# Optimization experiments

Hardware: AMD Instinct MI355X
Metric: run time of the kernel (lower is better)

## Reference

```python
import jax, jax.numpy as jnp
import numpy as np

EPS = 1e-05
NEG = -1e9

def rotate_half(x):
    x1, x2 = jnp.split(x, 2, axis=-1)
    return jnp.concatenate([-x2, x1], axis=-1)

def rmsnorm(x, w):
    xf = x.astype(jnp.float32)
    n = xf * jax.lax.rsqrt(jnp.mean(xf * xf, axis=-1, keepdims=True) + EPS)
    return w * n.astype(x.dtype)

def setup_inputs() -> dict:
    key = jax.random.key(0)
    ks = jax.random.split(key, 12)
    B, S, H, NH, DH, FF = 1, 2048, 2048, 16, 128, 8192
    x = jax.random.normal(ks[0], (B, S, H), jnp.float32)
    # additive causal mask [1,1,S,S]
    causal = jnp.where(jnp.tril(jnp.ones((S, S), bool)), 0.0, NEG).astype(jnp.float32)
    attention_mask = causal[None, None]
    alibi = 0.1 * jax.random.normal(ks[1], (1, NH, S, S), jnp.float32)
    # rotary angles [S, DH]
    inv = 1.0 / (10000.0 ** (jnp.arange(0, DH, 2, dtype=jnp.float32) / DH))
    ang = jnp.arange(S, dtype=jnp.float32)[:, None] * inv[None, :]
    freqs = jnp.concatenate([ang, ang], axis=-1)  # [S, DH]
    sc = 1.0 / np.sqrt(H)
    wq = sc * jax.random.normal(ks[2], (H, H), jnp.float32)
    wk = sc * jax.random.normal(ks[3], (H, H), jnp.float32)
    wv = sc * jax.random.normal(ks[4], (H, H), jnp.float32)
    wo = sc * jax.random.normal(ks[5], (H, H), jnp.float32)
    w1 = sc * jax.random.normal(ks[6], (H, FF), jnp.float32)
    w3 = sc * jax.random.normal(ks[7], (H, FF), jnp.float32)
    w2 = (1.0 / np.sqrt(FF)) * jax.random.normal(ks[8], (FF, H), jnp.float32)
    attn_norm_w = jnp.ones((H,), jnp.float32)
    ffn_norm_w = jnp.ones((H,), jnp.float32)
    return dict(x=x, attention_mask=attention_mask, alibi=alibi, freqs=freqs,
                wq=wq, wk=wk, wv=wv, wo=wo, w1=w1, w2=w2, w3=w3,
                attn_norm_w=attn_norm_w, ffn_norm_w=ffn_norm_w)

def reference(x, attention_mask, alibi, freqs, wq, wk, wv, wo, w1, w2, w3,
              attn_norm_w, ffn_norm_w):
    B, S, H = x.shape
    NH = 16
    DH = H // NH
    nx = rmsnorm(x, attn_norm_w)
    # projections -> [B, NH, S, DH]
    def heads(y):
        return y.reshape(B, S, NH, DH).transpose(0, 2, 1, 3)
    q = heads(nx @ wq)
    k = heads(nx @ wk)
    v = heads(nx @ wv)
    cos, sin = jnp.cos(freqs), jnp.sin(freqs)  # [S, DH] broadcasts over B,NH
    q = q * cos + rotate_half(q) * sin
    k = k * cos + rotate_half(k) * sin
    scores = jnp.einsum('bhqd,bhkd->bhqk', q, k) / np.sqrt(DH)
    scores = scores + attention_mask + alibi
    attn = jax.nn.softmax(scores, axis=-1)
    out = jnp.einsum('bhqk,bhkd->bhqd', attn, v)
    out = out.transpose(0, 2, 1, 3).reshape(B, S, H)
    x = x + out @ wo
    nx = rmsnorm(x, ffn_norm_w)
    ff = (jax.nn.silu(nx @ w1) * (nx @ w3)) @ w2
    return x + ff
```

## Files before the change

### kernel.cpp

```cpp
#include <hip/hip_runtime.h>
#include <hip/hip_bf16.h>
#include <math.h>

typedef __bf16 bf16x8 __attribute__((ext_vector_type(8)));
typedef float  f32x4  __attribute__((ext_vector_type(4)));
typedef unsigned short u16x8 __attribute__((ext_vector_type(8)));
typedef unsigned short u16x4 __attribute__((ext_vector_type(4)));

#define DEV static __device__ __forceinline__

DEV void gload16(const void* g, void* l) {
  __builtin_amdgcn_global_load_lds((__attribute__((address_space(1))) void*)g,
                                   (__attribute__((address_space(3))) void*)l,
                                   16, 0, 0);
}

DEV float bf2f(unsigned short u) {
  unsigned v = ((unsigned)u) << 16;
  return __builtin_bit_cast(float, v);
}
DEV unsigned short f2bf(float f) {
  unsigned u = __builtin_bit_cast(unsigned, f);
  u = u + 0x7fffu + ((u >> 16) & 1u);
  return (unsigned short)(u >> 16);
}

__global__ __launch_bounds__(256) void rmsnorm_k(const float* __restrict__ x,
    const float* __restrict__ w, unsigned short* __restrict__ out, int H) {
  int row = blockIdx.x;
  const float4* xr = (const float4*)(x + (size_t)row * H);
  float4 a = xr[threadIdx.x * 2], b = xr[threadIdx.x * 2 + 1];
  float ss = a.x*a.x + a.y*a.y + a.z*a.z + a.w*a.w
           + b.x*b.x + b.y*b.y + b.z*b.z + b.w*b.w;
#pragma unroll
  for (int o = 32; o; o >>= 1) ss += __shfl_down(ss, o, 64);
  __shared__ float red[4];
  if ((threadIdx.x & 63) == 0) red[threadIdx.x >> 6] = ss;
  __syncthreads();
  float rs = rsqrtf((red[0] + red[1] + red[2] + red[3]) * (1.0f / 2048.0f) + 1e-5f);
  size_t base = (size_t)row * H + threadIdx.x * 8;
  const float* wv = w + threadIdx.x * 8;
  float vals[8] = {a.x, a.y, a.z, a.w, b.x, b.y, b.z, b.w};
  u16x8 o8;
#pragma unroll
  for (int i = 0; i < 8; ++i) o8[i] = f2bf(vals[i] * rs * wv[i]);
  *(u16x8*)(out + base) = o8;
}

__global__ __launch_bounds__(256) void wtrans64_k(const float* __restrict__ W,
    unsigned short* __restrict__ Wt, int R, int C, int ilv) {
  __shared__ unsigned short tile[64][68];
  const int c0 = blockIdx.x * 64, r0 = blockIdx.y * 64;
  const int t = threadIdx.x;
  const int lr = t >> 4, lc4 = (t & 15) * 4;
#pragma unroll
  for (int i = 0; i < 4; ++i) {
    float4 v = *(const float4*)&W[(size_t)(r0 + lr + i * 16) * C + c0 + lc4];
    u16x4 s4;
    s4[0] = f2bf(v.x); s4[1] = f2bf(v.y); s4[2] = f2bf(v.z); s4[3] = f2bf(v.w);
    *(u16x4*)&tile[lr + i * 16][lc4] = s4;
  }
  __syncthreads();
  const int oc = t >> 3, seg = (t & 7) * 8;
#pragma unroll
  for (int i = 0; i < 2; ++i) {
    int c = c0 + oc + i * 32;
    u16x8 o8;
#pragma unroll
    for (int j = 0; j < 8; ++j) o8[j] = tile[seg + j][oc + i * 32];
    size_t dstrow = (ilv < 0) ? (size_t)c
                              : (size_t)(c >> 4) * 32 + (c & 15) + ilv * 16;
    *(u16x8*)&Wt[dstrow * R + r0 + seg] = o8;
  }
}


#define STG_A(H, BUF, KC) do {                                                 \
    gload16(Asrc0 + (size_t)(H) * 128 * lda + (KC),                            \
            &lds[(BUF) * 16384 + (H) * 8192 + w * 1024]);                      \
    gload16(Asrc1 + (size_t)(H) * 128 * lda + (KC),                            \
            &lds[(BUF) * 16384 + (H) * 8192 + w * 1024 + 512]);                \
  } while (0)

#define STG_B(H, BUF, KC) do {                                                 \
    gload16(Bsrc0 + (size_t)(H) * 128 * ldb + (KC),                            \
            &lds[32768 + (BUF) * 16384 + (H) * 8192 + w * 1024]);              \
    gload16(Bsrc1 + (size_t)(H) * 128 * ldb + (KC),                            \
            &lds[32768 + (BUF) * 16384 + (H) * 8192 + w * 1024 + 512]);        \
  } while (0)

#define DS_A(DST, MH) do {                                                     \
    const int abase = buf * 16384 + (MH) * 8192 + arow * 64;                   \
    _Pragma("unroll") for (int m = 0; m < 4; ++m) {                            \
      DST[m][0] = *(const bf16x8*)&lds[abase + m * 1024 + acol0];              \
      DST[m][1] = *(const bf16x8*)&lds[abase + m * 1024 + acol1];              \
    } } while (0)

#define DS_B(DST, NH) do {                                                     \
    const int bbase = 32768 + buf * 16384 + (NH) * 8192 + brow * 64;           \
    _Pragma("unroll") for (int n = 0; n < 2; ++n) {                            \
      DST[n][0] = *(const bf16x8*)&lds[bbase + n * 1024 + acol0];              \
      DST[n][1] = *(const bf16x8*)&lds[bbase + n * 1024 + acol1];              \
    } } while (0)

#define MFMA16(AI, AR, BR) do {                                                \
    _Pragma("unroll") for (int m = 0; m < 4; ++m)                              \
      _Pragma("unroll") for (int n = 0; n < 2; ++n) {                          \
        acc[AI][m][n] = __builtin_amdgcn_mfma_f32_16x16x32_bf16(               \
            AR[m][0], BR[n][0], acc[AI][m][n], 0, 0, 0);                       \
        acc[AI][m][n] = __builtin_amdgcn_mfma_f32_16x16x32_bf16(               \
            AR[m][1], BR[n][1], acc[AI][m][n], 0, 0, 0);                       \
      }                                                                        \
  } while (0)

template <int EPI>
__global__ __launch_bounds__(512, 2) void gemm256_k(
    const unsigned short* __restrict__ A, int lda,
    const unsigned short* __restrict__ B, int ldb,
    unsigned short* __restrict__ Cb, float* __restrict__ Cf,
    int M, int N, int Kext) {
  __shared__ unsigned short lds[65536];
  const int t = threadIdx.x, w = t >> 6, lane = t & 63;
  const int nbm = M >> 8, nbn = N >> 8, nwg = nbm * nbn;
  int id = blockIdx.x;
  id = (id & 7) * (nwg >> 3) + (id >> 3);
  const int bm = id % nbm, bn = id / nbm;
  const size_t m0 = (size_t)bm << 8, n0 = (size_t)bn << 8;
  const int koff = blockIdx.y * Kext;
  const int NT = Kext >> 6;
  const int scol = ((lane & 7) ^ (lane >> 3)) * 8;
  const unsigned short* Asrc0 = A + (m0 + w * 16 + (lane >> 3)) * (size_t)lda + koff + scol;
  const unsigned short* Asrc1 = A + (m0 + w * 16 + 8 + (lane >> 3)) * (size_t)lda + koff + scol;
  const unsigned short* Bsrc0 = B + (n0 + w * 16 + (lane >> 3)) * (size_t)ldb + koff + scol;
  const unsigned short* Bsrc1 = B + (n0 + w * 16 + 8 + (lane >> 3)) * (size_t)ldb + koff + scol;
  const int arow = (w >> 2) * 64 + (lane & 15);
  const int brow = (w & 3) * 32 + (lane & 15);
  const int acol0 = ((lane >> 4) * 8) ^ ((lane & 7) << 3);
  const int acol1 = acol0 ^ 32;
  f32x4 acc[4][4][2] = {};
  bf16x8 Acur[4][2], B0r[2][2], B1r[2][2];
  STG_A(0, 0, 0); STG_B(0, 0, 0); STG_A(1, 0, 0); STG_B(1, 0, 0);
  STG_A(0, 1, 64); STG_B(0, 1, 64);
  asm volatile("s_waitcnt vmcnt(4)" ::: "memory");
  __builtin_amdgcn_s_barrier();
  for (int kt = 0; kt < NT; ++kt) {
    const int buf = kt & 1;
    const int kc1 = (kt + 1) * 64, kc2 = (kt + 2) * 64;
    const bool p1 = (kt + 1 < NT), p2 = (kt + 2 < NT);
    DS_A(Acur, 0); DS_B(B0r, 0); DS_B(B1r, 1);
    if (p1) { STG_A(1, buf ^ 1, kc1); STG_B(1, buf ^ 1, kc1); }
    __builtin_amdgcn_sched_barrier(0);
    __builtin_amdgcn_s_barrier();
    __builtin_amdgcn_s_setprio(1);
    MFMA16(0, Acur, B0r);
    MFMA16(1, Acur, B1r);
    __builtin_amdgcn_s_setprio(0);
    __builtin_amdgcn_sched_barrier(0);
    __builtin_amdgcn_s_barrier();
    DS_A(Acur, 1);
    if (p2) { STG_A(0, buf, kc2); STG_B(0, buf, kc2); }
    __builtin_amdgcn_sched_barrier(0);
    __builtin_amdgcn_s_barrier();
    __builtin_amdgcn_s_setprio(1);
    MFMA16(2, Acur, B0r);
    MFMA16(3, Acur, B1r);
    __builtin_amdgcn_s_setprio(0);
    __builtin_amdgcn_sched_barrier(0);
    if (p2) { asm volatile("s_waitcnt vmcnt(4)" ::: "memory"); }
    else    { asm volatile("s_waitcnt vmcnt(0)" ::: "memory"); }
    __builtin_amdgcn_s_barrier();
  }
#pragma unroll
  for (int Mh = 0; Mh < 2; ++Mh)
#pragma unroll
    for (int Nh = 0; Nh < 2; ++Nh)
#pragma unroll
      for (int m = 0; m < 4; ++m) {
        size_t gr = m0 + Mh * 128 + (w >> 2) * 64 + m * 16 + (lane >> 4) * 4;
        if constexpr (EPI == 2) {
          size_t gc = (n0 >> 1) + Nh * 64 + (w & 3) * 16 + (lane & 15);
          f32x4 v0 = acc[Mh * 2 + Nh][m][0];
          f32x4 v1 = acc[Mh * 2 + Nh][m][1];
#pragma unroll
          for (int j = 0; j < 4; ++j) {
            float s = v0[j] / (1.0f + __expf(-v0[j]));
            Cb[(gr + j) * (size_t)(N >> 1) + gc] = f2bf(s * v1[j]);
          }
        } else {
#pragma unroll
          for (int n = 0; n < 2; ++n) {
            size_t gc = n0 + Nh * 128 + (w & 3) * 32 + n * 16 + (lane & 15);
            f32x4 v = acc[Mh * 2 + Nh][m][n];
#pragma unroll
            for (int j = 0; j < 4; ++j) {
              size_t o = (gr + j) * (size_t)N + gc;
              if constexpr (EPI == 0) Cb[o] = f2bf(v[j]);
              else Cf[(size_t)blockIdx.y * M * N + o] = v[j];
            }
          }
        }
      }
}

template <int EPI>
__global__ __launch_bounds__(256) void gemm_bt_k(
    const unsigned short* __restrict__ A, const unsigned short* __restrict__ B,
    float* __restrict__ Cf, unsigned short* __restrict__ Cb,
    const float* __restrict__ resid, int M, int N, int K) {
  constexpr int BK = 64;
  __shared__ unsigned short lA[128 * BK];
  __shared__ unsigned short lB[128 * BK];
  const int t = threadIdx.x, wave = t >> 6, lane = t & 63;
  int nwg = gridDim.x * gridDim.y;
  int id = blockIdx.y * gridDim.x + blockIdx.x;
  id = (id & 7) * (nwg >> 3) + (id >> 3);
  const int m0 = (id % gridDim.x) * 128, n0 = (id / gridDim.x) * 128;
  const int wr = (wave >> 1) * 64, wc = (wave & 1) * 64;
  f32x4 acc[4][4] = {};
  const int sr = t >> 3;
  const int sc = ((t & 7) ^ (sr & 7)) * 8;
  const unsigned short* Ab = A + (size_t)(m0 + sr) * K + sc;
  const unsigned short* Bb = B + (size_t)(n0 + sr) * K + sc;
  unsigned short* lAw = &lA[(wave * 8) * BK];
  unsigned short* lBw = &lB[(wave * 8) * BK];
  const int row = lane & 15, kg = (lane >> 4) * 8, swz = (lane & 7) << 3;
  for (int k0 = 0; k0 < K; k0 += BK) {
#pragma unroll
    for (int it = 0; it < 4; ++it) {
      gload16(Ab + (size_t)it * 32 * K + k0, lAw + it * 32 * BK);
      gload16(Bb + (size_t)it * 32 * K + k0, lBw + it * 32 * BK);
    }
    asm volatile("s_waitcnt vmcnt(0)" ::: "memory");
    __syncthreads();
#pragma unroll
    for (int kk = 0; kk < 2; ++kk) {
      bf16x8 af[4], bfr[4];
#pragma unroll
      for (int m = 0; m < 4; ++m)
        af[m] = *(const bf16x8*)&lA[(wr + m * 16 + row) * BK + ((kk * 32 + kg) ^ swz)];
#pragma unroll
      for (int n = 0; n < 4; ++n)
        bfr[n] = *(const bf16x8*)&lB[(wc + n * 16 + row) * BK + ((kk * 32 + kg) ^ swz)];
#pragma unroll
      for (int m = 0; m < 4; ++m)
#pragma unroll
        for (int n = 0; n < 4; ++n)
          acc[m][n] = __builtin_amdgcn_mfma_f32_16x16x32_bf16(af[m], bfr[n], acc[m][n], 0, 0, 0);
    }
    __syncthreads();
  }
  const int cg = lane >> 4, col = lane & 15;
#pragma unroll
  for (int m = 0; m < 4; ++m)
#pragma unroll
    for (int n = 0; n < 4; ++n) {
      int rr = m0 + wr + m * 16 + cg * 4;
      int cc = n0 + wc + n * 16 + col;
#pragma unroll
      for (int j = 0; j < 4; ++j) {
        float v = acc[m][n][j];
        size_t o = (size_t)(rr + j) * N + cc;
        if constexpr (EPI == 2) Cf[o] = v + resid[o];
        else if constexpr (EPI == 1) Cf[o] = v;
        else Cb[o] = f2bf(v);
      }
    }
}

__global__ __launch_bounds__(256) void rope_k(const unsigned short* __restrict__ qkv,
    const float* __restrict__ freqs, unsigned short* __restrict__ Qr,
    unsigned short* __restrict__ Kr, int S) {
  int idx = blockIdx.x * 256 + threadIdx.x;
  int dp = idx & 63, h = (idx >> 6) & 15, s = idx >> 10;
  float ang = freqs[s * 128 + dp];
  float c, sn;
  sincosf(ang, &sn, &c);
  size_t rq = (size_t)s * 6144 + h * 128 + dp;
  float q1 = bf2f(qkv[rq]),        q2 = bf2f(qkv[rq + 64]);
  float k1 = bf2f(qkv[rq + 2048]), k2 = bf2f(qkv[rq + 2048 + 64]);
  size_t ob = ((size_t)h * S + s) * 128 + dp;
  Qr[ob]      = f2bf(q1 * c - q2 * sn);
  Qr[ob + 64] = f2bf(q2 * c + q1 * sn);
  Kr[ob]      = f2bf(k1 * c - k2 * sn);
  Kr[ob + 64] = f2bf(k2 * c + k1 * sn);
}

__global__ __launch_bounds__(256) void vtrans_k(const unsigned short* __restrict__ qkv,
    unsigned short* __restrict__ Vt, int S) {
  __shared__ unsigned short tile[32][33];
  int h = blockIdx.z;
  int s0 = blockIdx.x * 32, d0 = blockIdx.y * 32;
  int tx = threadIdx.x, ty = threadIdx.y;
#pragma unroll
  for (int i = 0; i < 4; ++i)
    tile[ty + i * 8][tx] = qkv[(size_t)(s0 + ty + i * 8) * 6144 + 4096 + h * 128 + d0 + tx];
  __syncthreads();
#pragma unroll
  for (int i = 0; i < 4; ++i)
    Vt[((size_t)h * 128 + d0 + ty + i * 8) * S + s0 + tx] = tile[tx][ty + i * 8];
}

#define STGKV(KT, BUF) do {                                                    \
    _Pragma("unroll") for (int it = 0; it < 4; ++it)                           \
      gload16(Kb + (size_t)((KT) * 64 + it * 16 + sr) * 128 + scw,             \
              &lds[(BUF) * 8192 + (it * 16 + wave * 4) * 128]);                \
    _Pragma("unroll") for (int it = 0; it < 4; ++it)                           \
      gload16(Vb + (size_t)(it * 32 + vr) * S + (KT) * 64 + vcw,               \
              &lds[16384 + (BUF) * 8192 + (it * 32 + wave * 8) * 64]);         \
  } while (0)

#define ATTN_TILE(CUR, NXT, KT) do {                                           \
    const int buf = (KT) & 1;                                                  \
    const bool p1 = ((KT) + 1 < ktiles);                                       \
    if (p1) {                                                                  \
      STGKV((KT) + 1, buf ^ 1);                                                \
      _Pragma("unroll") for (int q8 = 0; q8 < 16; ++q8)                        \
        NXT[q8] = albase[(size_t)(q8 & 3) * S + ((KT) + 1) * 64 + (q8 >> 2) * 16]; \
      asm volatile("s_waitcnt vmcnt(24)" ::: "memory");                        \
    } else {                                                                   \
      asm volatile("s_waitcnt vmcnt(0)" ::: "memory");                         \
    }                                                                          \
    __builtin_amdgcn_s_barrier();                                              \
    f32x4 sf[4] = {};                                                          \
    _Pragma("unroll") for (int ks = 0; ks < 4; ++ks)                           \
      _Pragma("unroll") for (int n = 0; n < 4; ++n) {                          \
        bf16x8 kf = *(const bf16x8*)&lds[buf * 8192 + (n * 16 + row) * 128 +   \
                                         ((ks * 32 + kg) ^ kswz)];             \
        sf[n] = __builtin_amdgcn_mfma_f32_16x16x32_bf16(qf[ks], kf, sf[n], 0, 0, 0); \
      }                                                                        \
    float pv[4][4];                                                            \
    float tmax[4] = {-1e30f, -1e30f, -1e30f, -1e30f};                          \
    _Pragma("unroll") for (int n = 0; n < 4; ++n) {                            \
      int k_abs = (KT) * 64 + n * 16 + col;                                    \
      _Pragma("unroll") for (int j = 0; j < 4; ++j) {                          \
        int q_abs = q0 + wave * 16 + cg * 4 + j;                               \
        float v = sf[n][j] * scale + CUR[n * 4 + j];                           \
        if (k_abs > q_abs) v = -1e30f;                                         \
        pv[n][j] = v;                                                          \
        tmax[j] = fmaxf(tmax[j], v);                                           \
      } }                                                                      \
    _Pragma("unroll") for (int o2 = 1; o2 < 16; o2 <<= 1)                      \
      _Pragma("unroll") for (int j = 0; j < 4; ++j)                            \
        tmax[j] = fmaxf(tmax[j], __shfl_xor(tmax[j], o2, 64));                 \
    float alpha[4], rsum[4] = {};                                              \
    _Pragma("unroll") for (int j = 0; j < 4; ++j) {                            \
      float mn = fmaxf(m_run[j], tmax[j]);                                     \
      alpha[j] = __expf(m_run[j] - mn);                                        \
      m_run[j] = mn;                                                           \
    }                                                                          \
    _Pragma("unroll") for (int n = 0; n < 4; ++n)                              \
      _Pragma("unroll") for (int j = 0; j < 4; ++j) {                          \
        float p = __expf(pv[n][j] - m_run[j]);                                 \
        pv[n][j] = p;                                                          \
        rsum[j] += p;                                                          \
      }                                                                        \
    _Pragma("unroll") for (int o2 = 1; o2 < 16; o2 <<= 1)                      \
      _Pragma("unroll") for (int j = 0; j < 4; ++j)                            \
        rsum[j] += __shfl_xor(rsum[j], o2, 64);                                \
    _Pragma("unroll") for (int j = 0; j < 4; ++j)                              \
      l_run[j] = l_run[j] * alpha[j] + rsum[j];                                \
    _Pragma("unroll") for (int nn = 0; nn < 8; ++nn)                           \
      _Pragma("unroll") for (int j = 0; j < 4; ++j) o[nn][j] *= alpha[j];      \
    _Pragma("unroll") for (int n = 0; n < 4; ++n)                              \
      _Pragma("unroll") for (int j = 0; j < 4; ++j) {                          \
        int pr = cg * 4 + j;                                                   \
        pw[pr * 64 + ((n * 16 + col) ^ ((pr & 7) << 3))] = f2bf(pv[n][j]);     \
      }                                                                        \
    asm volatile("s_waitcnt lgkmcnt(0)" ::: "memory");                         \
    __builtin_amdgcn_sched_barrier(0);                                         \
    _Pragma("unroll") for (int kk = 0; kk < 2; ++kk) {                         \
      bf16x8 pf = *(const bf16x8*)&pw[row * 64 + ((kk * 32 + kg) ^ kswz)];     \
      _Pragma("unroll") for (int nn = 0; nn < 8; ++nn) {                       \
        bf16x8 vf = *(const bf16x8*)&lds[16384 + buf * 8192 +                  \
                                         (nn * 16 + row) * 64 +                \
                                         ((kk * 32 + kg) ^ kswz)];             \
        o[nn] = __builtin_amdgcn_mfma_f32_16x16x32_bf16(pf, vf, o[nn], 0, 0, 0); \
      } }                                                                      \
    __builtin_amdgcn_s_barrier();                                              \
  } while (0)

__global__ __launch_bounds__(256) void attn_k(
    const unsigned short* __restrict__ Qr, const unsigned short* __restrict__ Kr,
    const unsigned short* __restrict__ Vt, const float* __restrict__ alibi,
    unsigned short* __restrict__ Ao, int S) {
  __shared__ unsigned short lds[36864];
  const int t = threadIdx.x, wave = t >> 6, lane = t & 63;
  const int h = blockIdx.y, nq = gridDim.x, bx = blockIdx.x;
  const int qt = (bx & 1) ? (nq - 1 - (bx >> 1)) : (bx >> 1);
  const int q0 = qt * 64;
  const int sr = t >> 4, scw = ((t & 15) ^ ((t >> 4) & 7)) * 8;
  const int vr = t >> 3, vcw = ((t & 7) ^ ((t >> 3) & 7)) * 8;
  const unsigned short* Kb = Kr + (size_t)h * S * 128;
  const unsigned short* Vb = Vt + (size_t)h * 128 * S;
  const int row = lane & 15, kg = (lane >> 4) * 8, cg = lane >> 4, col = lane & 15;
  const int kswz = (lane & 7) << 3;
  bf16x8 qf[4];
  const unsigned short* Qrow = Qr + ((size_t)h * S + q0 + wave * 16 + row) * 128;
#pragma unroll
  for (int ks = 0; ks < 4; ++ks) qf[ks] = *(const bf16x8*)&Qrow[ks * 32 + kg];
  f32x4 o[8] = {};
  float m_run[4] = {-1e30f, -1e30f, -1e30f, -1e30f};
  float l_run[4] = {};
  unsigned short* pw = &lds[32768 + wave * 1024];
  const float scale = 0.08838834764831843f;
  const int ktiles = qt + 1;
  const float* albase = alibi + (size_t)h * S * S +
                        ((size_t)q0 + wave * 16 + cg * 4) * S + col;
  float alA[16], alB[16];
  STGKV(0, 0);
#pragma unroll
  for (int q8 = 0; q8 < 16; ++q8)
    alA[q8] = albase[(size_t)(q8 & 3) * S + (q8 >> 2) * 16];
  for (int kt = 0; kt < ktiles; kt += 2) {
    ATTN_TILE(alA, alB, kt);
    if (kt + 1 < ktiles) ATTN_TILE(alB, alA, kt + 1);
  }
#pragma unroll
  for (int nn = 0; nn < 8; ++nn)
#pragma unroll
    for (int j = 0; j < 4; ++j) {
      int q_abs = q0 + wave * 16 + cg * 4 + j;
      Ao[(size_t)q_abs * 2048 + h * 128 + nn * 16 + col] = f2bf(o[nn][j] / l_run[j]);
    }
}

__global__ __launch_bounds__(256) void reduce4_k(const float* __restrict__ part,
    const float* __restrict__ resid, float* __restrict__ out, int n4, size_t mn) {
  int i = blockIdx.x * 256 + threadIdx.x;
  if (i >= n4) return;
  const float4* p = (const float4*)part;
  size_t q = mn >> 2;
  float4 a = ((const float4*)resid)[i];
  float4 s0 = p[i], s1 = p[i + q], s2 = p[i + 2 * q], s3 = p[i + 3 * q];
  float4 r;
  r.x = a.x + s0.x + s1.x + s2.x + s3.x;
  r.y = a.y + s0.y + s1.y + s2.y + s3.y;
  r.z = a.z + s0.z + s1.z + s2.z + s3.z;
  r.w = a.w + s0.w + s1.w + s2.w + s3.w;
  ((float4*)out)[i] = r;
}

extern "C" void kernel_launch(void* const* d_in, const int* in_sizes, int n_in,
                              void* d_out, int out_size, void* d_ws, size_t ws_size,
                              hipStream_t stream) {
  const int S = 2048, H = 2048, NH = 16, DH = 128, FF = 8192;
  const float* x     = (const float*)d_in[0];
  const float* alibi = (const float*)d_in[2];
  const float* freqs = (const float*)d_in[3];
  const float* wq    = (const float*)d_in[4];
  const float* wk    = (const float*)d_in[5];
  const float* wv    = (const float*)d_in[6];
  const float* wo    = (const float*)d_in[7];
  const float* w1    = (const float*)d_in[8];
  const float* w2    = (const float*)d_in[9];
  const float* w3    = (const float*)d_in[10];
  const float* anw   = (const float*)d_in[11];
  const float* fnw   = (const float*)d_in[12];
  float* out = (float*)d_out;

  char* ws = (char*)d_ws;
  size_t off = 0;
  auto alloc = [&](size_t n) { char* p = ws + off; off += (n + 255) & ~(size_t)255; return p; };
  unsigned short* qkvT = (unsigned short*)alloc((size_t)3 * H * H * 2);
  unsigned short* woT  = (unsigned short*)alloc((size_t)H * H * 2);
  unsigned short* w13T = (unsigned short*)alloc((size_t)2 * FF * H * 2);
  unsigned short* w2T  = (unsigned short*)alloc((size_t)H * FF * 2);
  float*          x2   = (float*)alloc((size_t)S * H * 4);
  unsigned short* nx2  = (unsigned short*)alloc((size_t)S * H * 2);
  unsigned short* gbuf = (unsigned short*)alloc((size_t)S * FF * 2);
  unsigned short* nx   = (unsigned short*)alloc((size_t)S * H * 2);
  unsigned short* qkvb = (unsigned short*)alloc((size_t)S * 3 * H * 2);
  unsigned short* Qr   = (unsigned short*)alloc((size_t)NH * S * DH * 2);
  unsigned short* Kr   = (unsigned short*)alloc((size_t)NH * S * DH * 2);
  unsigned short* Vt   = (unsigned short*)alloc((size_t)NH * DH * S * 2);
  unsigned short* attno= (unsigned short*)alloc((size_t)S * H * 2);
  float* part = (float*)ws;

  dim3 tb32(32, 8);
  wtrans64_k<<<dim3(32, 32), 256, 0, stream>>>(wq, qkvT, H, H, -1);
  wtrans64_k<<<dim3(32, 32), 256, 0, stream>>>(wk, qkvT + (size_t)H * H, H, H, -1);
  wtrans64_k<<<dim3(32, 32), 256, 0, stream>>>(wv, qkvT + (size_t)2 * H * H, H, H, -1);
  wtrans64_k<<<dim3(32, 32), 256, 0, stream>>>(wo, woT, H, H, -1);
  wtrans64_k<<<dim3(128, 32), 256, 0, stream>>>(w1, w13T, H, FF, 0);
  wtrans64_k<<<dim3(128, 32), 256, 0, stream>>>(w3, w13T, H, FF, 1);
  wtrans64_k<<<dim3(32, 128), 256, 0, stream>>>(w2, w2T, FF, H, -1);

  rmsnorm_k<<<S, 256, 0, stream>>>(x, anw, nx, H);
  gemm256_k<0><<<dim3(192, 1), 512, 0, stream>>>(nx, H, qkvT, H, qkvb, nullptr, S, 3 * H, H);
  rope_k<<<(S * NH * 64) / 256, 256, 0, stream>>>(qkvb, freqs, Qr, Kr, S);
  vtrans_k<<<dim3(S / 32, DH / 32, NH), tb32, 0, stream>>>(qkvb, Vt, S);
  attn_k<<<dim3(S / 64, NH), 256, 0, stream>>>(Qr, Kr, Vt, alibi, attno, S);
  gemm_bt_k<2><<<dim3(16, 16), 256, 0, stream>>>(attno, woT, x2, nullptr, x, S, H, H);
  rmsnorm_k<<<S, 256, 0, stream>>>(x2, fnw, nx2, H);
  gemm256_k<2><<<dim3(512, 1), 512, 0, stream>>>(nx2, H, w13T, H, gbuf, nullptr, S, 2 * FF, H);
  gemm256_k<1><<<dim3(64, 4), 512, 0, stream>>>(gbuf, FF, w2T, FF, nullptr, part, S, H, H);
  reduce4_k<<<4096, 256, 0, stream>>>(part, x2, out, S * H / 4, (size_t)S * H);
}
```

Before: 535.7 us.

## Restructure 256x256 GEMM to BK=32 triple-buffered LDS pipeline with 128x64 warp tiles

```diff
diff --git a/kernel.cpp b/kernel.cpp
--- a/kernel.cpp
+++ b/kernel.cpp
@@ -75,42 +75,16 @@
 }
 
 
-#define STG_A(H, BUF, KC) do {                                                 \
-    gload16(Asrc0 + (size_t)(H) * 128 * lda + (KC),                            \
-            &lds[(BUF) * 16384 + (H) * 8192 + w * 1024]);                      \
-    gload16(Asrc1 + (size_t)(H) * 128 * lda + (KC),                            \
-            &lds[(BUF) * 16384 + (H) * 8192 + w * 1024 + 512]);                \
+#define STG_A32(BUF, KC) do {                                                  \
+    gload16(Asrc + (KC), &lds[(BUF) * 16384 + t * 8]);                         \
+    gload16(Asrc + (size_t)128 * lda + (KC),                                   \
+            &lds[(BUF) * 16384 + 4096 + t * 8]);                               \
   } while (0)
 
-#define STG_B(H, BUF, KC) do {                                                 \
-    gload16(Bsrc0 + (size_t)(H) * 128 * ldb + (KC),                            \
-            &lds[32768 + (BUF) * 16384 + (H) * 8192 + w * 1024]);              \
-    gload16(Bsrc1 + (size_t)(H) * 128 * ldb + (KC),                            \
-            &lds[32768 + (BUF) * 16384 + (H) * 8192 + w * 1024 + 512]);        \
-  } while (0)
-
-#define DS_A(DST, MH) do {                                                     \
-    const int abase = buf * 16384 + (MH) * 8192 + arow * 64;                   \
-    _Pragma("unroll") for (int m = 0; m < 4; ++m) {                            \
-      DST[m][0] = *(const bf16x8*)&lds[abase + m * 1024 + acol0];              \
-      DST[m][1] = *(const bf16x8*)&lds[abase + m * 1024 + acol1];              \
-    } } while (0)
-
-#define DS_B(DST, NH) do {                                                     \
-    const int bbase = 32768 + buf * 16384 + (NH) * 8192 + brow * 64;           \
-    _Pragma("unroll") for (int n = 0; n < 2; ++n) {                            \
-      DST[n][0] = *(const bf16x8*)&lds[bbase + n * 1024 + acol0];              \
-      DST[n][1] = *(const bf16x8*)&lds[bbase + n * 1024 + acol1];              \
-    } } while (0)
-
-#define MFMA16(AI, AR, BR) do {                                                \
-    _Pragma("unroll") for (int m = 0; m < 4; ++m)                              \
-      _Pragma("unroll") for (int n = 0; n < 2; ++n) {                          \
-        acc[AI][m][n] = __builtin_amdgcn_mfma_f32_16x16x32_bf16(               \
-            AR[m][0], BR[n][0], acc[AI][m][n], 0, 0, 0);                       \
-        acc[AI][m][n] = __builtin_amdgcn_mfma_f32_16x16x32_bf16(               \
-            AR[m][1], BR[n][1], acc[AI][m][n], 0, 0, 0);                       \
-      }                                                                        \
+#define STG_B32(BUF, KC) do {                                                  \
+    gload16(Bsrc + (KC), &lds[(BUF) * 16384 + 8192 + t * 8]);                  \
+    gload16(Bsrc + (size_t)128 * ldb + (KC),                                   \
+            &lds[(BUF) * 16384 + 12288 + t * 8]);                              \
   } while (0)
 
 template <int EPI>
@@ -119,7 +93,7 @@
     const unsigned short* __restrict__ B, int ldb,
     unsigned short* __restrict__ Cb, float* __restrict__ Cf,
     int M, int N, int Kext) {
-  __shared__ unsigned short lds[65536];
+  __shared__ unsigned short lds[49152];
   const int t = threadIdx.x, w = t >> 6, lane = t & 63;
   const int nbm = M >> 8, nbn = N >> 8, nwg = nbm * nbn;
   int id = blockIdx.x;
@@ -127,79 +101,74 @@
   const int bm = id % nbm, bn = id / nbm;
   const size_t m0 = (size_t)bm << 8, n0 = (size_t)bn << 8;
   const int koff = blockIdx.y * Kext;
-  const int NT = Kext >> 6;
-  const int scol = ((lane & 7) ^ (lane >> 3)) * 8;
-  const unsigned short* Asrc0 = A + (m0 + w * 16 + (lane >> 3)) * (size_t)lda + koff + scol;
-  const unsigned short* Asrc1 = A + (m0 + w * 16 + 8 + (lane >> 3)) * (size_t)lda + koff + scol;
-  const unsigned short* Bsrc0 = B + (n0 + w * 16 + (lane >> 3)) * (size_t)ldb + koff + scol;
-  const unsigned short* Bsrc1 = B + (n0 + w * 16 + 8 + (lane >> 3)) * (size_t)ldb + koff + scol;
-  const int arow = (w >> 2) * 64 + (lane & 15);
-  const int brow = (w & 3) * 32 + (lane & 15);
-  const int acol0 = ((lane >> 4) * 8) ^ ((lane & 7) << 3);
-  const int acol1 = acol0 ^ 32;
-  f32x4 acc[4][4][2] = {};
-  bf16x8 Acur[4][2], B0r[2][2], B1r[2][2];
-  STG_A(0, 0, 0); STG_B(0, 0, 0); STG_A(1, 0, 0); STG_B(1, 0, 0);
-  STG_A(0, 1, 64); STG_B(0, 1, 64);
+  const int NT = Kext >> 5;
+  const int scol = ((t & 3) ^ ((t >> 2) & 3)) * 8;
+  const unsigned short* Asrc = A + (m0 + (t >> 2)) * (size_t)lda + koff + scol;
+  const unsigned short* Bsrc = B + (n0 + (t >> 2)) * (size_t)ldb + koff + scol;
+  const int wm = w >> 2, wn = w & 3;
+  const int acol = ((lane >> 4) ^ (lane & 3)) * 8;
+  const int arow0 = wm * 128 + (lane & 15);
+  const int brow0 = wn * 64 + (lane & 15);
+  f32x4 acc[8][4] = {};
+  STG_A32(0, 0); STG_B32(0, 0);
+  STG_A32(1, 32); STG_B32(1, 32);
   asm volatile("s_waitcnt vmcnt(4)" ::: "memory");
   __builtin_amdgcn_s_barrier();
+  int b = 0, b2 = 2;
   for (int kt = 0; kt < NT; ++kt) {
-    const int buf = kt & 1;
-    const int kc1 = (kt + 1) * 64, kc2 = (kt + 2) * 64;
-    const bool p1 = (kt + 1 < NT), p2 = (kt + 2 < NT);
-    DS_A(Acur, 0); DS_B(B0r, 0); DS_B(B1r, 1);
-    if (p1) { STG_A(1, buf ^ 1, kc1); STG_B(1, buf ^ 1, kc1); }
-    __builtin_amdgcn_sched_barrier(0);
+    if (kt + 2 < NT) {
+      const int kc2 = (kt + 2) * 32;
+      STG_A32(b2, kc2); STG_B32(b2, kc2);
+    }
+    const int abase = b * 16384 + arow0 * 32 + acol;
+    const int bbase = b * 16384 + 8192 + brow0 * 32 + acol;
+    bf16x8 bfr[4];
+#pragma unroll
+    for (int fn = 0; fn < 4; ++fn)
+      bfr[fn] = *(const bf16x8*)&lds[bbase + fn * 512];
+    __builtin_amdgcn_s_setprio(1);
+#pragma unroll
+    for (int fr = 0; fr < 8; ++fr) {
+      bf16x8 af = *(const bf16x8*)&lds[abase + fr * 512];
+#pragma unroll
+      for (int fn = 0; fn < 4; ++fn)
+        acc[fr][fn] = __builtin_amdgcn_mfma_f32_16x16x32_bf16(af, bfr[fn], acc[fr][fn], 0, 0, 0);
+    }
+    __builtin_amdgcn_s_setprio(0);
+    if (kt + 2 < NT)      { asm volatile("s_waitcnt vmcnt(4)" ::: "memory"); }
+    else if (kt + 1 < NT) { asm volatile("s_waitcnt vmcnt(0)" ::: "memory"); }
     __builtin_amdgcn_s_barrier();
-    __builtin_amdgcn_s_setprio(1);
-    MFMA16(0, Acur, B0r);
-    MFMA16(1, Acur, B1r);
-    __builtin_amdgcn_s_setprio(0);
-    __builtin_amdgcn_sched_barrier(0);
-    __builtin_amdgcn_s_barrier();
-    DS_A(Acur, 1);
-    if (p2) { STG_A(0, buf, kc2); STG_B(0, buf, kc2); }
-    __builtin_amdgcn_sched_barrier(0);
-    __builtin_amdgcn_s_barrier();
-    __builtin_amdgcn_s_setprio(1);
-    MFMA16(2, Acur, B0r);
-    MFMA16(3, Acur, B1r);
-    __builtin_amdgcn_s_setprio(0);
-    __builtin_amdgcn_sched_barrier(0);
-    if (p2) { asm volatile("s_waitcnt vmcnt(4)" ::: "memory"); }
-    else    { asm volatile("s_waitcnt vmcnt(0)" ::: "memory"); }
-    __builtin_amdgcn_s_barrier();
-  }
-#pragma unroll
-  for (int Mh = 0; Mh < 2; ++Mh)
-#pragma unroll
-    for (int Nh = 0; Nh < 2; ++Nh)
-#pragma unroll
-      for (int m = 0; m < 4; ++m) {
-        size_t gr = m0 + Mh * 128 + (w >> 2) * 64 + m * 16 + (lane >> 4) * 4;
-        if constexpr (EPI == 2) {
-          size_t gc = (n0 >> 1) + Nh * 64 + (w & 3) * 16 + (lane & 15);
-          f32x4 v0 = acc[Mh * 2 + Nh][m][0];
-          f32x4 v1 = acc[Mh * 2 + Nh][m][1];
-#pragma unroll
-          for (int j = 0; j < 4; ++j) {
-            float s = v0[j] / (1.0f + __expf(-v0[j]));
-            Cb[(gr + j) * (size_t)(N >> 1) + gc] = f2bf(s * v1[j]);
-          }
-        } else {
-#pragma unroll
-          for (int n = 0; n < 2; ++n) {
-            size_t gc = n0 + Nh * 128 + (w & 3) * 32 + n * 16 + (lane & 15);
-            f32x4 v = acc[Mh * 2 + Nh][m][n];
-#pragma unroll
-            for (int j = 0; j < 4; ++j) {
-              size_t o = (gr + j) * (size_t)N + gc;
-              if constexpr (EPI == 0) Cb[o] = f2bf(v[j]);
-              else Cf[(size_t)blockIdx.y * M * N + o] = v[j];
-            }
-          }
+    b = (b == 2) ? 0 : b + 1;
+    b2 = (b2 == 2) ? 0 : b2 + 1;
+  }
+#pragma unroll
+  for (int fr = 0; fr < 8; ++fr) {
+    size_t gr = m0 + wm * 128 + fr * 16 + (lane >> 4) * 4;
+    if constexpr (EPI == 2) {
+#pragma unroll
+      for (int p = 0; p < 2; ++p) {
+        f32x4 v0 = acc[fr][2 * p], v1 = acc[fr][2 * p + 1];
+        size_t gc = (n0 >> 1) + (wn * 2 + p) * 16 + (lane & 15);
+#pragma unroll
+        for (int j = 0; j < 4; ++j) {
+          float s = v0[j] / (1.0f + __expf(-v0[j]));
+          Cb[(gr + j) * (size_t)(N >> 1) + gc] = f2bf(s * v1[j]);
         }
       }
+    } else {
+#pragma unroll
+      for (int fn = 0; fn < 4; ++fn) {
+        size_t gc = n0 + wn * 64 + fn * 16 + (lane & 15);
+        f32x4 v = acc[fr][fn];
+#pragma unroll
+        for (int j = 0; j < 4; ++j) {
+          size_t o = (gr + j) * (size_t)N + gc;
+          if constexpr (EPI == 0) Cb[o] = f2bf(v[j]);
+          else Cf[(size_t)blockIdx.y * M * N + o] = v[j];
+        }
+      }
+    }
+  }
 }
 
 template <int EPI>
```

Result: slower. 554.6 us (+3.5%).
